# Kernel tuning notes

Hardware: AMD Instinct MI355X
Metric: run time of the kernel (lower is better)

## Reference

```python
import jax, jax.numpy as jnp
import numpy as np
from jax import lax

FIRE_RATE = 0.5
N_CHANNELS = 16
HIDDEN = 128


def _sobel_kernels():
    # Replicates NCAModel3D.sobel_filter_3d, expressed directly in the
    # channels-last (S1,S2,S3) layout used below. Torch builds kernels,
    # permutes them (1,2,0), then applies them after x.transpose(1,4);
    # composing the two permutations, the effective kernels in our layout
    # are exactly the pre-permute tensors: kx[k,i,j] = w[k]*w[i]*d[j].
    w = np.array([1.0, 2.0, 1.0], np.float32)
    d = np.array([-1.0, 0.0, 1.0], np.float32)
    kx = w[:, None, None] * w[None, :, None] * d[None, None, :]  # [3,3,3]
    kx = kx / np.abs(kx).sum()
    ky = kx.transpose(0, 2, 1)
    kz = kx.transpose(2, 1, 0)
    return jnp.asarray(kx), jnp.asarray(ky), jnp.asarray(kz)


KX, KY, KZ = _sobel_kernels()


def _dwconv(x, k):
    # depthwise 3x3x3 conv (cross-correlation, matching F.conv3d), SAME padding
    c = x.shape[-1]
    ker = jnp.broadcast_to(k[:, :, :, None, None], (3, 3, 3, 1, c))  # DHWIO
    return lax.conv_general_dilated(
        x, ker, window_strides=(1, 1, 1), padding='SAME',
        dimension_numbers=('NDHWC', 'DHWIO', 'NDHWC'),
        feature_group_count=c)


def _alive(x):
    # max_pool3d(kernel=3, stride=1, pad=1) on alpha channel (index 3) > 0.1
    a = lax.reduce_window(x[..., 3:4], -jnp.inf, lax.max,
                          (1, 3, 3, 3, 1), (1, 1, 1, 1, 1), 'SAME')
    return a > 0.1


def setup_inputs() -> dict:
    key = jax.random.key(0)
    k1, k2, k3, k4, k5 = jax.random.split(key, 5)
    B, S = 4, 64
    x = jax.random.uniform(k1, (B, S, S, S, N_CHANNELS), dtype=jnp.float32)
    w0 = jax.random.normal(k2, (HIDDEN, 4 * N_CHANNELS), dtype=jnp.float32) * 0.05
    b0 = jax.random.normal(k3, (HIDDEN,), dtype=jnp.float32) * 0.05
    # torch zero-inits fc1; use small random weights so the output is non-trivial
    w1 = jax.random.normal(k4, (N_CHANNELS, HIDDEN), dtype=jnp.float32) * 0.05
    stoch = jax.random.uniform(k5, (B, S, S, S, 1), dtype=jnp.float32)
    return {'x': x, 'w0': w0, 'b0': b0, 'w1': w1, 'stoch': stoch}


def reference(x, w0, b0, w1, stoch):
    # one NCA update step (steps=1)
    pre_life = _alive(x)                                        # [B,S,S,S,1] bool
    y = jnp.concatenate(
        [x, _dwconv(x, KX), _dwconv(x, KY), _dwconv(x, KZ)], axis=-1)  # [B,S,S,S,4C]
    h = jax.nn.relu(jnp.einsum('bdhwc,kc->bdhwk', y, w0) + b0)  # fc0 + relu
    dx = jnp.einsum('bdhwk,ck->bdhwc', h, w1)                   # fc1 (no bias)
    dx = dx * (stoch > FIRE_RATE)                               # stochastic mask
    x2 = x + dx
    life = (pre_life & _alive(x2)).astype(x.dtype)
    return x2 * life
```

## Files before the change

kernel.cpp:

```cpp
#include <hip/hip_runtime.h>
#include <hip/hip_bf16.h>

typedef unsigned short u16t;
typedef __attribute__((ext_vector_type(8))) short short8;
typedef __attribute__((ext_vector_type(8))) unsigned short ushort8;
typedef __attribute__((ext_vector_type(4))) unsigned short ushort4v;
typedef __attribute__((ext_vector_type(4))) float f32x4;

#define VTOT 1048576

__device__ __forceinline__ float bf2f(u16t u) {
  union { unsigned int i; float f; } v; v.i = ((unsigned int)u) << 16; return v.f;
}
__device__ __forceinline__ u16t f2bf(float f) {
  __hip_bfloat16 h = __float2bfloat16(f);
  union { __hip_bfloat16 b; u16t u; } v; v.b = h; return v.u;
}

__global__ __launch_bounds__(256, 2) void nca_main(
    const float* __restrict__ xg, const float* __restrict__ w0g,
    const float* __restrict__ b0g, const float* __restrict__ w1g,
    const float* __restrict__ stg, float* __restrict__ outg,
    float* __restrict__ aws, unsigned char* __restrict__ plife)
{
  __shared__ u16t smem[34816];
  __shared__ float st_l[256];
  __shared__ float alpha_l[256];
  __shared__ unsigned char pl_l[256];

  const int t = threadIdx.x;
  const int bid = blockIdx.x;
  const int b = bid >> 10;
  const int z1base = ((bid >> 5) & 31) * 2;
  const int z2base = (bid & 31) * 2;
  const int YO = 16896;

  {
    int z1 = t >> 7, z2 = (t >> 6) & 1, z3 = t & 63;
    int gv = ((b * 64 + z1base + z1) * 64 + (z2base + z2)) * 64 + z3;
    st_l[t] = stg[gv];
  }

  for (int it = 0; it < 17; ++it) {
    int q = t + it * 256;
    if (q < 4224) {
      int c4 = (q & 3) * 4, s = q >> 2;
      int i3 = s % 66, r = s / 66;
      int i2 = r & 3, i1 = r >> 2;
      int z1g = z1base + i1 - 1, z2g = z2base + i2 - 1, z3g = i3 - 1;
      f32x4 val = {0.f, 0.f, 0.f, 0.f};
      if ((unsigned)z1g < 64u && (unsigned)z2g < 64u && (unsigned)z3g < 64u) {
        int gv = ((b * 64 + z1g) * 64 + z2g) * 64 + z3g;
        val = *(const f32x4*)(xg + gv * 16 + c4);
      }
      ushort4v bv;
      #pragma unroll
      for (int j = 0; j < 4; ++j) bv[j] = f2bf(val[j]);
      *(ushort4v*)(smem + s * 16 + c4) = bv;
    }
  }
  __syncthreads();

  {
    const int hc = t & 1, vq = t >> 1;
    const int z2 = (vq >> 6) & 1, z3 = vq & 63;
    float axA[8], ayA[8], azA[8], axB[8], ayB[8], azB[8];
    #pragma unroll
    for (int c = 0; c < 8; ++c) {
      axA[c] = 0.f; ayA[c] = 0.f; azA[c] = 0.f;
      axB[c] = 0.f; ayB[c] = 0.f; azB[c] = 0.f;
    }
    ushort8 ctrA{}, ctrB{};
    float amaxA = 0.0f, amaxB = 0.0f;
    const float W[3] = {1.f, 2.f, 1.f};
    const float D[3] = {-1.f, 0.f, 1.f};
    #pragma unroll
    for (int d1 = 0; d1 < 3; ++d1)
      #pragma unroll
      for (int d2 = 0; d2 < 3; ++d2)
        #pragma unroll
        for (int d3 = 0; d3 < 3; ++d3) {
          const int rowA = ((0 + d1) * 4 + (z2 + d2)) * 66 + (z3 + d3);
          ushort8 uA = *(const ushort8*)(smem + rowA * 16 + hc * 8);
          ushort8 uB = *(const ushort8*)(smem + (rowA + 264) * 16 + hc * 8);
          float fA[8], fB[8];
          #pragma unroll
          for (int c = 0; c < 8; ++c) { fA[c] = bf2f((u16t)uA[c]); fB[c] = bf2f((u16t)uB[c]); }
          const float cx = W[d1] * W[d2] * D[d3] * 0.03125f;
          const float cy = W[d1] * D[d2] * W[d3] * 0.03125f;
          const float cz = D[d1] * W[d2] * W[d3] * 0.03125f;
          if (cx != 0.f) {
            #pragma unroll
            for (int c = 0; c < 8; ++c) {
              axA[c] = fmaf(fA[c], cx, axA[c]); axB[c] = fmaf(fB[c], cx, axB[c]);
            }
          }
          if (cy != 0.f) {
            #pragma unroll
            for (int c = 0; c < 8; ++c) {
              ayA[c] = fmaf(fA[c], cy, ayA[c]); ayB[c] = fmaf(fB[c], cy, ayB[c]);
            }
          }
          if (cz != 0.f) {
            #pragma unroll
            for (int c = 0; c < 8; ++c) {
              azA[c] = fmaf(fA[c], cz, azA[c]); azB[c] = fmaf(fB[c], cz, azB[c]);
            }
          }
          if (d1 == 1 && d2 == 1 && d3 == 1) { ctrA = uA; ctrB = uB; }
          amaxA = fmaxf(amaxA, fA[3]);
          amaxB = fmaxf(amaxB, fB[3]);
        }
    *(ushort8*)(smem + YO + (0 + hc) * 2048 + vq * 8) = ctrA;
    *(ushort8*)(smem + YO + (0 + hc) * 2048 + (vq + 128) * 8) = ctrB;
    ushort8 bxA, byA, bzA, bxB, byB, bzB;
    #pragma unroll
    for (int c = 0; c < 8; ++c) {
      bxA[c] = (short)f2bf(axA[c]); byA[c] = (short)f2bf(ayA[c]); bzA[c] = (short)f2bf(azA[c]);
      bxB[c] = (short)f2bf(axB[c]); byB[c] = (short)f2bf(ayB[c]); bzB[c] = (short)f2bf(azB[c]);
    }
    *(ushort8*)(smem + YO + (2 + hc) * 2048 + vq * 8) = bxA;
    *(ushort8*)(smem + YO + (4 + hc) * 2048 + vq * 8) = byA;
    *(ushort8*)(smem + YO + (6 + hc) * 2048 + vq * 8) = bzA;
    *(ushort8*)(smem + YO + (2 + hc) * 2048 + (vq + 128) * 8) = bxB;
    *(ushort8*)(smem + YO + (4 + hc) * 2048 + (vq + 128) * 8) = byB;
    *(ushort8*)(smem + YO + (6 + hc) * 2048 + (vq + 128) * 8) = bzB;
    if (hc == 0) {
      pl_l[vq] = (amaxA > 0.1f) ? (unsigned char)1 : (unsigned char)0;
      pl_l[vq + 128] = (amaxB > 0.1f) ? (unsigned char)1 : (unsigned char)0;
    }
  }

  const int lane = t & 63, w = t >> 6;
  const int col = lane & 15, quad = lane >> 4;
  short8 w0f[2][2];
  #pragma unroll
  for (int kt = 0; kt < 2; ++kt)
    #pragma unroll
    for (int nt = 0; nt < 2; ++nt) {
      const float* pw = w0g + (w * 32 + nt * 16 + col) * 64 + kt * 32 + quad * 8;
      f32x4 lo = *(const f32x4*)pw, hi = *(const f32x4*)(pw + 4);
      short8 fr;
      #pragma unroll
      for (int j = 0; j < 4; ++j) { fr[j] = (short)f2bf(lo[j]); fr[4 + j] = (short)f2bf(hi[j]); }
      w0f[kt][nt] = fr;
    }
  f32x4 biasv[2];
  #pragma unroll
  for (int nt = 0; nt < 2; ++nt)
    biasv[nt] = *(const f32x4*)(b0g + w * 32 + nt * 16 + quad * 4);

  __syncthreads();

  {
    ushort4v hpk[8][2];

    #pragma unroll
    for (int mt = 0; mt < 8; ++mt) {
      short8 yf[2];
      #pragma unroll
      for (int kt = 0; kt < 2; ++kt)
        yf[kt] = *(const short8*)(smem + YO + (kt * 4 + quad) * 2048 + (mt * 16 + col) * 8);
      f32x4 acc[2];
      acc[0] = biasv[0]; acc[1] = biasv[1];
      #pragma unroll
      for (int kt = 0; kt < 2; ++kt)
        #pragma unroll
        for (int nt = 0; nt < 2; ++nt)
          acc[nt] = __builtin_amdgcn_mfma_f32_16x16x32_bf16(w0f[kt][nt], yf[kt], acc[nt], 0, 0, 0);
      #pragma unroll
      for (int nt = 0; nt < 2; ++nt) {
        ushort4v hv;
        #pragma unroll
        for (int r = 0; r < 4; ++r) hv[r] = f2bf(fmaxf(acc[nt][r], 0.0f));
        hpk[mt][nt] = hv;
      }
    }
    __syncthreads();
    #pragma unroll
    for (int mt = 0; mt < 8; ++mt)
      #pragma unroll
      for (int nt = 0; nt < 2; ++nt)
        *(ushort4v*)(smem + (mt * 16 + col) * 136 + w * 32 + nt * 16 + quad * 4) = hpk[mt][nt];

    #pragma unroll
    for (int mt = 0; mt < 8; ++mt) {
      short8 yf[2];
      #pragma unroll
      for (int kt = 0; kt < 2; ++kt)
        yf[kt] = *(const short8*)(smem + YO + (kt * 4 + quad) * 2048 + (128 + mt * 16 + col) * 8);
      f32x4 acc[2];
      acc[0] = biasv[0]; acc[1] = biasv[1];
      #pragma unroll
      for (int kt = 0; kt < 2; ++kt)
        #pragma unroll
        for (int nt = 0; nt < 2; ++nt)
          acc[nt] = __builtin_amdgcn_mfma_f32_16x16x32_bf16(w0f[kt][nt], yf[kt], acc[nt], 0, 0, 0);
      #pragma unroll
      for (int nt = 0; nt < 2; ++nt) {
        ushort4v hv;
        #pragma unroll
        for (int r = 0; r < 4; ++r) hv[r] = f2bf(fmaxf(acc[nt][r], 0.0f));
        hpk[mt][nt] = hv;
      }
    }

    short8 w1f[4];
    #pragma unroll
    for (int kt = 0; kt < 4; ++kt) {
      const float* pw = w1g + col * 128 + kt * 32 + quad * 8;
      f32x4 lo = *(const f32x4*)pw, hi = *(const f32x4*)(pw + 4);
      short8 fr;
      #pragma unroll
      for (int j = 0; j < 4; ++j) { fr[j] = (short)f2bf(lo[j]); fr[4 + j] = (short)f2bf(hi[j]); }
      w1f[kt] = fr;
    }

    __syncthreads();
    #pragma unroll
    for (int mt = 0; mt < 8; ++mt)
      #pragma unroll
      for (int nt = 0; nt < 2; ++nt)
        *(ushort4v*)(smem + (128 + mt * 16 + col) * 136 + w * 32 + nt * 16 + quad * 4) = hpk[mt][nt];
    __syncthreads();

    #pragma unroll
    for (int mt2 = 0; mt2 < 4; ++mt2) {
      const int mbase = w * 64 + mt2 * 16;
      f32x4 dxa = {0.f, 0.f, 0.f, 0.f};
      #pragma unroll
      for (int kt = 0; kt < 4; ++kt) {
        short8 ah = *(const short8*)(smem + (mbase + col) * 136 + kt * 32 + quad * 8);
        dxa = __builtin_amdgcn_mfma_f32_16x16x32_bf16(ah, w1f[kt], dxa, 0, 0, 0);
      }
      #pragma unroll
      for (int r = 0; r < 4; ++r) {
        const int v = mbase + quad * 4 + r;
        const int z1 = v >> 7, z2 = (v >> 6) & 1, z3 = v & 63;
        const int gv = ((b * 64 + z1base + z1) * 64 + (z2base + z2)) * 64 + z3;
        const int addr = gv * 16 + col;
        float dx = (st_l[v] > 0.5f) ? dxa[r] : 0.0f;
        float x2 = xg[addr] + dx;
        outg[addr] = x2;
        if (col == 3) alpha_l[v] = x2;
      }
    }
  }
  __syncthreads();
  if (aws != nullptr) {
    const int v = t, z3 = t & 63;
    const float a = alpha_l[v];
    const float up = (z3 > 0) ? alpha_l[v - 1] : -1e30f;
    const float dn = (z3 < 63) ? alpha_l[v + 1] : -1e30f;
    const int gv = ((b * 64 + z1base + (v >> 7)) * 64 + (z2base + ((v >> 6) & 1))) * 64 + z3;
    aws[gv] = fmaxf(a, fmaxf(up, dn));
    plife[gv] = pl_l[v];
  }
}

__global__ void nca_life(const float* __restrict__ aws,
                         const unsigned char* __restrict__ plife,
                         float* __restrict__ og)
{
  __shared__ float m3s[2304];
  const int t = threadIdx.x, bid = blockIdx.x;
  const int b = bid >> 8;
  const int z1b = ((bid >> 4) & 15) * 4;
  const int z2b = (bid & 15) * 4;
  #pragma unroll
  for (int it = 0; it < 9; ++it) {
    const int q = t + it * 256;
    const int row = q >> 6, z3 = q & 63;
    const int r1 = z1b + (row / 6) - 1, r2 = z2b + (row % 6) - 1;
    float a = -1e30f;
    if ((unsigned)r1 < 64u && (unsigned)r2 < 64u)
      a = aws[((b * 64 + r1) * 64 + r2) * 64 + z3];
    m3s[q] = a;
  }
  unsigned char pl[4]; int gvs[4];
  #pragma unroll
  for (int k = 0; k < 4; ++k) {
    const int v = t + k * 256;
    const int z1l = v >> 8, z2l = (v >> 6) & 3, z3 = v & 63;
    gvs[k] = ((b * 64 + z1b + z1l) * 64 + (z2b + z2l)) * 64 + z3;
    pl[k] = plife[gvs[k]];
  }
  __syncthreads();
  #pragma unroll
  for (int k = 0; k < 4; ++k) {
    const int v = t + k * 256;
    const int z1l = v >> 8, z2l = (v >> 6) & 3, z3 = v & 63;
    float mo = -1e30f;
    #pragma unroll
    for (int d1 = 0; d1 < 3; ++d1)
      #pragma unroll
      for (int d2 = 0; d2 < 3; ++d2)
        mo = fmaxf(mo, m3s[((z1l + d1) * 6 + (z2l + d2)) * 64 + z3]);
    const bool life = (pl[k] != 0) && (mo > 0.1f);
    if (!life) {
      f32x4 z = {0.f, 0.f, 0.f, 0.f};
      #pragma unroll
      for (int j = 0; j < 4; ++j) *(f32x4*)(og + gvs[k] * 16 + j * 4) = z;
    }
  }
}

__global__ void nca_life_strided(const float* __restrict__ xg, const float* __restrict__ outg,
                                 float* __restrict__ og)
{
  __shared__ float a2x[1056];
  __shared__ float a2o[1056];
  const int t = threadIdx.x, bid = blockIdx.x;
  const int b = bid >> 10;
  const int z1base = ((bid >> 5) & 31) * 2;
  const int z2base = (bid & 31) * 2;
  for (int it = 0; it < 5; ++it) {
    int q = t + it * 256;
    if (q < 1056) {
      int i3 = q % 66, r = q / 66;
      int i2 = r & 3, i1 = r >> 2;
      int z1g = z1base + i1 - 1, z2g = z2base + i2 - 1, z3g = i3 - 1;
      float vx = 0.f, vo = 0.f;
      if ((unsigned)z1g < 64u && (unsigned)z2g < 64u && (unsigned)z3g < 64u) {
        int gv = ((b * 64 + z1g) * 64 + z2g) * 64 + z3g;
        vx = xg[gv * 16 + 3];
        vo = outg[gv * 16 + 3];
      }
      a2x[q] = vx; a2o[q] = vo;
    }
  }
  __syncthreads();
  const int z1 = t >> 7, z2 = (t >> 6) & 1, z3 = t & 63;
  float mx = -1e30f, mo = -1e30f;
  #pragma unroll
  for (int d1 = 0; d1 < 3; ++d1)
    #pragma unroll
    for (int d2 = 0; d2 < 3; ++d2)
      #pragma unroll
      for (int d3 = 0; d3 < 3; ++d3) {
        const int idx = ((z1 + d1) * 4 + (z2 + d2)) * 66 + (z3 + d3);
        mx = fmaxf(mx, a2x[idx]);
        mo = fmaxf(mo, a2o[idx]);
      }
  const bool life = (mx > 0.1f) && (mo > 0.1f);
  if (!life) {
    const int gv = ((b * 64 + z1base + z1) * 64 + (z2base + z2)) * 64 + z3;
    f32x4 z = {0.f, 0.f, 0.f, 0.f};
    #pragma unroll
    for (int j = 0; j < 4; ++j) *(f32x4*)(og + gv * 16 + j * 4) = z;
  }
}

extern "C" void kernel_launch(void* const* d_in, const int* in_sizes, int n_in,
                              void* d_out, int out_size, void* d_ws, size_t ws_size,
                              hipStream_t stream) {
  (void)out_size;
  const void *px = nullptr, *pw0 = nullptr, *pb0 = nullptr, *pw1 = nullptr, *pst = nullptr;
  for (int i = 0; i < n_in; ++i) {
    switch (in_sizes[i]) {
      case 16777216: px  = d_in[i]; break;
      case 8192:     pw0 = d_in[i]; break;
      case 128:      pb0 = d_in[i]; break;
      case 2048:     pw1 = d_in[i]; break;
      case 1048576:  pst = d_in[i]; break;
    }
  }
  if (!px || !pw0 || !pb0 || !pw1 || !pst) {
    px = d_in[0]; pw0 = d_in[1]; pb0 = d_in[2]; pw1 = d_in[3]; pst = d_in[4];
  }
  float* outg = (float*)d_out;
  const size_t need = (size_t)VTOT * 4 + (size_t)VTOT;
  const bool use_ws = (d_ws != nullptr) && (ws_size >= need);
  float* aws = use_ws ? (float*)d_ws : nullptr;
  unsigned char* plife = use_ws ? ((unsigned char*)d_ws + (size_t)VTOT * 4) : nullptr;

  nca_main<<<4096, 256, 0, stream>>>((const float*)px, (const float*)pw0, (const float*)pb0,
                                     (const float*)pw1, (const float*)pst, outg, aws, plife);
  if (use_ws)
    nca_life<<<1024, 256, 0, stream>>>(aws, plife, outg);
  else
    nca_life_strided<<<4096, 256, 0, stream>>>((const float*)px, outg, outg);
}
```

Measured before the change: 242.8 us.

## Vectorize halo load, prefetch x residual, drop a barrier, retune LDS stride

The halo fill now uses 8 fixed iterations. Each thread loads 32 contiguous bytes along z3 with no div/mod index math, and the z3 edge rows are zero-filled separately. The x values for the residual add are prefetched into registers before the final barrier, so their global-load latency overlaps the hidden-layer LDS writes. One __syncthreads before the first h store is removed, and the h-tile row stride goes from 136 to 132 elements, shrinking LDS use. This risks a race if the removed barrier was protecting the overlap with the halo region, and the new stride may change bank-conflict behaviour.

```diff
diff --git a/kernel.cpp b/kernel.cpp
--- a/kernel.cpp
+++ b/kernel.cpp
@@ -23,7 +23,7 @@
     const float* __restrict__ stg, float* __restrict__ outg,
     float* __restrict__ aws, unsigned char* __restrict__ plife)
 {
-  __shared__ u16t smem[34816];
+  __shared__ u16t smem[33792];
   __shared__ float st_l[256];
   __shared__ float alpha_l[256];
   __shared__ unsigned char pl_l[256];
@@ -41,23 +41,27 @@
     st_l[t] = stg[gv];
   }
 
-  for (int it = 0; it < 17; ++it) {
-    int q = t + it * 256;
-    if (q < 4224) {
-      int c4 = (q & 3) * 4, s = q >> 2;
-      int i3 = s % 66, r = s / 66;
-      int i2 = r & 3, i1 = r >> 2;
-      int z1g = z1base + i1 - 1, z2g = z2base + i2 - 1, z3g = i3 - 1;
-      f32x4 val = {0.f, 0.f, 0.f, 0.f};
-      if ((unsigned)z1g < 64u && (unsigned)z2g < 64u && (unsigned)z3g < 64u) {
-        int gv = ((b * 64 + z1g) * 64 + z2g) * 64 + z3g;
-        val = *(const f32x4*)(xg + gv * 16 + c4);
-      }
-      ushort4v bv;
-      #pragma unroll
-      for (int j = 0; j < 4; ++j) bv[j] = f2bf(val[j]);
-      *(ushort4v*)(smem + s * 16 + c4) = bv;
-    }
+  #pragma unroll
+  for (int it = 0; it < 8; ++it) {
+    const int row = it * 2 + (t >> 7);
+    const int z3g = (t >> 1) & 63;
+    const int half = t & 1;
+    const int z1g = z1base + (row >> 2) - 1, z2g = z2base + (row & 3) - 1;
+    f32x4 v0 = {0.f, 0.f, 0.f, 0.f}, v1 = {0.f, 0.f, 0.f, 0.f};
+    if ((unsigned)z1g < 64u && (unsigned)z2g < 64u) {
+      const float* p = xg + ((((b * 64 + z1g) * 64 + z2g) * 64 + z3g) * 16) + half * 8;
+      v0 = *(const f32x4*)p;
+      v1 = *(const f32x4*)(p + 4);
+    }
+    ushort8 pk;
+    #pragma unroll
+    for (int j = 0; j < 4; ++j) { pk[j] = f2bf(v0[j]); pk[4 + j] = f2bf(v1[j]); }
+    *(ushort8*)(smem + (row * 66 + z3g + 1) * 16 + half * 8) = pk;
+  }
+  if (t < 64) {
+    const int row = t >> 2, edge = (t >> 1) & 1, half = t & 1;
+    ushort8 z{};
+    *(ushort8*)(smem + (row * 66 + edge * 65) * 16 + half * 8) = z;
   }
   __syncthreads();
 
@@ -116,8 +120,8 @@
     ushort8 bxA, byA, bzA, bxB, byB, bzB;
     #pragma unroll
     for (int c = 0; c < 8; ++c) {
-      bxA[c] = (short)f2bf(axA[c]); byA[c] = (short)f2bf(ayA[c]); bzA[c] = (short)f2bf(azA[c]);
-      bxB[c] = (short)f2bf(axB[c]); byB[c] = (short)f2bf(ayB[c]); bzB[c] = (short)f2bf(azB[c]);
+      bxA[c] = f2bf(axA[c]); byA[c] = f2bf(ayA[c]); bzA[c] = f2bf(azA[c]);
+      bxB[c] = f2bf(axB[c]); byB[c] = f2bf(ayB[c]); bzB[c] = f2bf(azB[c]);
     }
     *(ushort8*)(smem + YO + (2 + hc) * 2048 + vq * 8) = bxA;
     *(ushort8*)(smem + YO + (4 + hc) * 2048 + vq * 8) = byA;
@@ -176,12 +180,11 @@
         hpk[mt][nt] = hv;
       }
     }
-    __syncthreads();
     #pragma unroll
     for (int mt = 0; mt < 8; ++mt)
       #pragma unroll
       for (int nt = 0; nt < 2; ++nt)
-        *(ushort4v*)(smem + (mt * 16 + col) * 136 + w * 32 + nt * 16 + quad * 4) = hpk[mt][nt];
+        *(ushort4v*)(smem + (mt * 16 + col) * 132 + w * 32 + nt * 16 + quad * 4) = hpk[mt][nt];
 
     #pragma unroll
     for (int mt = 0; mt < 8; ++mt) {
@@ -205,6 +208,17 @@
       }
     }
 
+    float xv[16];
+    #pragma unroll
+    for (int mt2 = 0; mt2 < 4; ++mt2)
+      #pragma unroll
+      for (int r = 0; r < 4; ++r) {
+        const int v = w * 64 + mt2 * 16 + quad * 4 + r;
+        const int z1 = v >> 7, z2 = (v >> 6) & 1, z3 = v & 63;
+        const int gv = ((b * 64 + z1base + z1) * 64 + (z2base + z2)) * 64 + z3;
+        xv[mt2 * 4 + r] = xg[gv * 16 + col];
+      }
+
     short8 w1f[4];
     #pragma unroll
     for (int kt = 0; kt < 4; ++kt) {
@@ -221,7 +235,7 @@
     for (int mt = 0; mt < 8; ++mt)
       #pragma unroll
       for (int nt = 0; nt < 2; ++nt)
-        *(ushort4v*)(smem + (128 + mt * 16 + col) * 136 + w * 32 + nt * 16 + quad * 4) = hpk[mt][nt];
+        *(ushort4v*)(smem + (128 + mt * 16 + col) * 132 + w * 32 + nt * 16 + quad * 4) = hpk[mt][nt];
     __syncthreads();
 
     #pragma unroll
@@ -230,7 +244,7 @@
       f32x4 dxa = {0.f, 0.f, 0.f, 0.f};
       #pragma unroll
       for (int kt = 0; kt < 4; ++kt) {
-        short8 ah = *(const short8*)(smem + (mbase + col) * 136 + kt * 32 + quad * 8);
+        short8 ah = *(const short8*)(smem + (mbase + col) * 132 + kt * 32 + quad * 8);
         dxa = __builtin_amdgcn_mfma_f32_16x16x32_bf16(ah, w1f[kt], dxa, 0, 0, 0);
       }
       #pragma unroll
@@ -240,7 +254,7 @@
         const int gv = ((b * 64 + z1base + z1) * 64 + (z2base + z2)) * 64 + z3;
         const int addr = gv * 16 + col;
         float dx = (st_l[v] > 0.5f) ? dxa[r] : 0.0f;
-        float x2 = xg[addr] + dx;
+        float x2 = xv[mt2 * 4 + r] + dx;
         outg[addr] = x2;
         if (col == 3) alpha_l[v] = x2;
       }
```

After: 202.1 us. 1.2x faster.
